# Kernel tuning notes

Measured on AMD Instinct MI355X. Metric: run time of the kernel, lower is better.

## Reference

```python
import jax, jax.numpy as jnp
import numpy as np

N = 100000   # nodes
E = 1600000  # edges (avg degree ~16)
DIN, DH, DOUT = 128, 128, 32
EPS = 1e-5


def setup_inputs() -> dict:
    key = jax.random.key(0)
    ks = jax.random.split(key, 6)
    x = jax.random.normal(ks[0], (N, DIN), jnp.float32)
    edge_index = jax.random.randint(ks[1], (2, E), 0, N, dtype=jnp.int64)

    def w(k, i, o):
        return jax.random.normal(k, (i, o), jnp.float32) * (1.0 / np.sqrt(i))

    return dict(
        x=x, edge_index=edge_index,
        W0=w(ks[2], DIN, DH), b0=jnp.zeros((DH,), jnp.float32),
        g0=jnp.ones((DH,), jnp.float32), be0=jnp.zeros((DH,), jnp.float32),
        W1=w(ks[3], DH, DH), b1=jnp.zeros((DH,), jnp.float32),
        g1=jnp.ones((DH,), jnp.float32), be1=jnp.zeros((DH,), jnp.float32),
        W2=w(ks[4], DH, DOUT), b2=jnp.zeros((DOUT,), jnp.float32),
    )


def _gcn_conv(x, src, dst, norm, W, b, n):
    # x' = scatter_add_dst( norm * (x W)[src] ) + b   (PyG GCNConv, self-loops in src/dst)
    h = x @ W
    out = jax.ops.segment_sum(h[src] * norm[:, None], dst, num_segments=n)
    return out + b


def _bn(x, g, b):
    # training-mode BatchNorm1d over the node axis (biased variance)
    m = x.mean(axis=0)
    v = jnp.mean((x - m) ** 2, axis=0)
    return (x - m) * jax.lax.rsqrt(v + EPS) * g + b


def reference(x, edge_index, W0, b0, g0, be0, W1, b1, g1, be1, W2, b2):
    n = x.shape[0]
    loops = jnp.arange(n, dtype=edge_index.dtype)
    src = jnp.concatenate([edge_index[0], loops])
    dst = jnp.concatenate([edge_index[1], loops])
    # symmetric degree normalization: deg computed on destination with self-loops
    deg = jax.ops.segment_sum(jnp.ones_like(dst, dtype=x.dtype), dst, num_segments=n)
    dinv = jnp.where(deg > 0, jax.lax.rsqrt(jnp.maximum(deg, 1.0)), 0.0)
    norm = dinv[src] * dinv[dst]  # [E+N]

    h = _gcn_conv(x, src, dst, norm, W0, b0, n)
    h = jax.nn.relu(_bn(h, g0, be0))  # dropout is identity at eval
    h = _gcn_conv(h, src, dst, norm, W1, b1, n)
    h = jax.nn.relu(_bn(h, g1, be1))
    h = _gcn_conv(h, src, dst, norm, W2, b2, n)
    return jax.nn.log_softmax(h, axis=1)
```

## Files before the change

kernel.cpp:

```cpp
#include <hip/hip_runtime.h>
#include <hip/hip_bf16.h>
#include <cstdint>
#include <cstddef>

#define BN_EPS 1e-5f

__global__ void detect_k(const int* __restrict__ edges, int* __restrict__ flag) {
    int t = threadIdx.x;
    int v = edges[2 * t + 1];
    unsigned long long b = __ballot(v == 0);
    if (t == 0) flag[0] = (b == ~0ULL) ? 1 : 0;
}

__global__ void init_k(int* __restrict__ cnt, float* __restrict__ stats, int n) {
    int i = blockIdx.x * 256 + threadIdx.x;
    if (i < n) cnt[i] = 0;
    if (i < 1024) stats[i] = 0.0f;
}

__global__ void convert_count_k(const void* __restrict__ edges, int E, const int* __restrict__ flag,
                                int* __restrict__ src32, int* __restrict__ dst32,
                                int* __restrict__ ord, int* __restrict__ cnt) {
    int e = blockIdx.x * 256 + threadIdx.x;
    if (e >= E) return;
    int s, d;
    if (flag[0]) {
        const long long* p = (const long long*)edges;
        s = (int)p[e]; d = (int)p[(size_t)E + e];
    } else {
        const int* p = (const int*)edges;
        s = p[e]; d = p[(size_t)E + e];
    }
    src32[e] = s; dst32[e] = d;
    ord[e] = atomicAdd(&cnt[d], 1);
}

__global__ __launch_bounds__(256) void scan1_k(const int* __restrict__ cnt,
                                               int* __restrict__ stmp,
                                               int* __restrict__ bsum, int n) {
    __shared__ int lds[256];
    int t = threadIdx.x, b = blockIdx.x;
    int base = b * 1024 + t * 4;
    int v0 = (base + 0 < n) ? cnt[base + 0] : 0;
    int v1 = (base + 1 < n) ? cnt[base + 1] : 0;
    int v2 = (base + 2 < n) ? cnt[base + 2] : 0;
    int v3 = (base + 3 < n) ? cnt[base + 3] : 0;
    int p0 = v0, p1 = p0 + v1, p2 = p1 + v2, p3 = p2 + v3;
    lds[t] = p3;
    __syncthreads();
    int own = p3;
    for (int o = 1; o < 256; o <<= 1) {
        int x = (t >= o) ? lds[t - o] : 0;
        __syncthreads();
        lds[t] += x;
        __syncthreads();
    }
    int excl = lds[t] - own;
    if (base + 0 < n) stmp[base + 0] = excl + p0;
    if (base + 1 < n) stmp[base + 1] = excl + p1;
    if (base + 2 < n) stmp[base + 2] = excl + p2;
    if (base + 3 < n) stmp[base + 3] = excl + p3;
    if (t == 255) bsum[b] = lds[255];
}

__global__ void scan2_k(int* __restrict__ bsum, int nb) {
    __shared__ int lds[128];
    int t = threadIdx.x;
    int v = (t < nb) ? bsum[t] : 0;
    lds[t] = v;
    __syncthreads();
    for (int o = 1; o < 128; o <<= 1) {
        int x = (t >= o) ? lds[t - o] : 0;
        __syncthreads();
        lds[t] += x;
        __syncthreads();
    }
    if (t < nb) bsum[t] = lds[t] - v;
}

__global__ void scan3_k(const int* __restrict__ cnt, const int* __restrict__ stmp,
                        const int* __restrict__ bsum, int* __restrict__ rowptr,
                        float* __restrict__ dinv, int n, int E) {
    int i = blockIdx.x * 256 + threadIdx.x;
    if (i < n) {
        rowptr[i] = stmp[i] - cnt[i] + bsum[i >> 10];
        dinv[i] = rsqrtf((float)(cnt[i] + 1));
    }
    if (i == 0) rowptr[n] = E;
}

__global__ void fill_k(const int* __restrict__ src32, const int* __restrict__ dst32,
                       const int* __restrict__ ord, const int* __restrict__ rowptr,
                       const float* __restrict__ dinv,
                       int2* __restrict__ csre, int E) {
    int e = blockIdx.x * 256 + threadIdx.x;
    if (e >= E) return;
    int s = src32[e], d = dst32[e];
    int slot = rowptr[d] + ord[e];
    float w = dinv[s] * dinv[d];
    csre[slot] = make_int2(s, __float_as_int(w));
}

__device__ inline unsigned pack_bf16(float a, float b) {
    unsigned ua = __float_as_uint(a);
    unsigned ub = __float_as_uint(b);
    ua += 0x7FFFu + ((ua >> 16) & 1u);
    ub += 0x7FFFu + ((ub >> 16) & 1u);
    return (ua >> 16) | (ub & 0xFFFF0000u);
}

__device__ inline void unp_bf16(unsigned u, float& a, float& b) {
    a = __uint_as_float(u << 16);
    b = __uint_as_float(u & 0xFFFF0000u);
}

template <int NCOL, bool FUSE_BN, bool OUT_BF16>
__global__ __launch_bounds__(256) void gemm_k(const float* __restrict__ X,
                                              const float* __restrict__ W,
                                              void* __restrict__ Yv, int nrows,
                                              const float* __restrict__ stats,
                                              const float* __restrict__ gam,
                                              const float* __restrict__ bet) {
    constexpr int KDIM = 128;
    constexpr int TM = 64;
    constexpr int KT = 32;
    constexpr int CPT = NCOL / 16;
    __shared__ float xt[KDIM][TM + 4];
    __shared__ float wt[KT][NCOL];

    const int t = threadIdx.x;
    const int ty = t >> 4, tx = t & 15;
    const int row0 = blockIdx.x * TM;

    float sc[4], sh[4];
    if (FUSE_BN) {
        float invn = 1.0f / (float)nrows;
        int k4c = (t & 31) * 4;
#pragma unroll
        for (int j = 0; j < 4; ++j) {
            int c = k4c + j;
            float m = stats[c] * invn;
            float var = stats[128 + c] * invn - m * m;
            float s = rsqrtf(var + BN_EPS) * gam[c];
            sc[j] = s;
            sh[j] = bet[c] - m * s;
        }
    }

    const float4* X4 = (const float4*)X;
#pragma unroll
    for (int i = 0; i < 8; ++i) {
        int idx = i * 256 + t;
        int r = idx >> 5;
        int k4 = idx & 31;
        int gr = row0 + r;
        if (gr > nrows - 1) gr = nrows - 1;
        float4 v = X4[(size_t)gr * 32 + k4];
        if (FUSE_BN) {
            v.x = fmaxf(fmaf(v.x, sc[0], sh[0]), 0.0f);
            v.y = fmaxf(fmaf(v.y, sc[1], sh[1]), 0.0f);
            v.z = fmaxf(fmaf(v.z, sc[2], sh[2]), 0.0f);
            v.w = fmaxf(fmaf(v.w, sc[3], sh[3]), 0.0f);
        }
        xt[k4 * 4 + 0][r] = v.x;
        xt[k4 * 4 + 1][r] = v.y;
        xt[k4 * 4 + 2][r] = v.z;
        xt[k4 * 4 + 3][r] = v.w;
    }

    int colIdx[CPT];
#pragma unroll
    for (int c = 0; c < CPT; ++c)
        colIdx[c] = OUT_BF16 ? (2 * tx + (c & 1) + 32 * (c >> 1)) : (tx + 16 * c);

    float acc[4][CPT];
#pragma unroll
    for (int r = 0; r < 4; ++r)
#pragma unroll
        for (int c = 0; c < CPT; ++c) acc[r][c] = 0.0f;

    const float4* W4 = (const float4*)W;
    for (int kt = 0; kt < KDIM / KT; ++kt) {
        __syncthreads();
        constexpr int F4 = KT * NCOL / 4;
#pragma unroll
        for (int i = 0; i < F4 / 256; ++i) {
            int idx = i * 256 + t;
            int r = idx / (NCOL / 4);
            int c4 = idx % (NCOL / 4);
            float4 v = W4[(size_t)(kt * KT + r) * (NCOL / 4) + c4];
            *(float4*)&wt[r][c4 * 4] = v;
        }
        __syncthreads();
#pragma unroll
        for (int k = 0; k < KT; ++k) {
            float4 a = *(const float4*)&xt[kt * KT + k][ty * 4];
            float av[4] = {a.x, a.y, a.z, a.w};
            float bv[CPT];
#pragma unroll
            for (int c = 0; c < CPT; ++c) bv[c] = wt[k][colIdx[c]];
#pragma unroll
            for (int r = 0; r < 4; ++r)
#pragma unroll
                for (int c = 0; c < CPT; ++c)
                    acc[r][c] = fmaf(av[r], bv[c], acc[r][c]);
        }
    }

#pragma unroll
    for (int r = 0; r < 4; ++r) {
        int gr = row0 + ty * 4 + r;
        if (gr < nrows) {
            if (OUT_BF16) {
                unsigned* Y16 = (unsigned*)Yv;
#pragma unroll
                for (int c2 = 0; c2 < CPT / 2; ++c2)
                    Y16[(size_t)gr * (NCOL / 2) + tx + 16 * c2] =
                        pack_bf16(acc[r][2 * c2], acc[r][2 * c2 + 1]);
            } else {
                float* Y = (float*)Yv;
#pragma unroll
                for (int c = 0; c < CPT; ++c)
                    Y[(size_t)gr * NCOL + tx + 16 * c] = acc[r][c];
            }
        }
    }
}

__global__ __launch_bounds__(256) void agg16_k(const unsigned* __restrict__ H16,
                                               const float* __restrict__ dinv,
                                               const int* __restrict__ rowptr,
                                               const int2* __restrict__ csre,
                                               const float* __restrict__ bias,
                                               float* __restrict__ out, int n) {
    int g = threadIdx.x >> 4;
    int lane = threadIdx.x & 15;
    int node = blockIdx.x * 16 + g;
    if (node >= n) return;

    const uint4* H4 = (const uint4*)H16;
    float di = dinv[node];
    float w0 = di * di;
    float acc[8];
    {
        uint4 sv = H4[(size_t)node * 16 + lane];
        float a, b;
        unp_bf16(sv.x, a, b); acc[0] = w0 * a; acc[1] = w0 * b;
        unp_bf16(sv.y, a, b); acc[2] = w0 * a; acc[3] = w0 * b;
        unp_bf16(sv.z, a, b); acc[4] = w0 * a; acc[5] = w0 * b;
        unp_bf16(sv.w, a, b); acc[6] = w0 * a; acc[7] = w0 * b;
    }

    int s = rowptr[node], e = rowptr[node + 1];
    for (; s + 1 < e; s += 2) {
        int2 ev0 = csre[s];
        int2 ev1 = csre[s + 1];
        uint4 h0 = H4[(size_t)ev0.x * 16 + lane];
        uint4 h1 = H4[(size_t)ev1.x * 16 + lane];
        float wa = __int_as_float(ev0.y);
        float wb = __int_as_float(ev1.y);
        float a, b;
        unp_bf16(h0.x, a, b); acc[0] = fmaf(wa, a, acc[0]); acc[1] = fmaf(wa, b, acc[1]);
        unp_bf16(h0.y, a, b); acc[2] = fmaf(wa, a, acc[2]); acc[3] = fmaf(wa, b, acc[3]);
        unp_bf16(h0.z, a, b); acc[4] = fmaf(wa, a, acc[4]); acc[5] = fmaf(wa, b, acc[5]);
        unp_bf16(h0.w, a, b); acc[6] = fmaf(wa, a, acc[6]); acc[7] = fmaf(wa, b, acc[7]);
        unp_bf16(h1.x, a, b); acc[0] = fmaf(wb, a, acc[0]); acc[1] = fmaf(wb, b, acc[1]);
        unp_bf16(h1.y, a, b); acc[2] = fmaf(wb, a, acc[2]); acc[3] = fmaf(wb, b, acc[3]);
        unp_bf16(h1.z, a, b); acc[4] = fmaf(wb, a, acc[4]); acc[5] = fmaf(wb, b, acc[5]);
        unp_bf16(h1.w, a, b); acc[6] = fmaf(wb, a, acc[6]); acc[7] = fmaf(wb, b, acc[7]);
    }
    if (s < e) {
        int2 ev = csre[s];
        uint4 hv = H4[(size_t)ev.x * 16 + lane];
        float w = __int_as_float(ev.y);
        float a, b;
        unp_bf16(hv.x, a, b); acc[0] = fmaf(w, a, acc[0]); acc[1] = fmaf(w, b, acc[1]);
        unp_bf16(hv.y, a, b); acc[2] = fmaf(w, a, acc[2]); acc[3] = fmaf(w, b, acc[3]);
        unp_bf16(hv.z, a, b); acc[4] = fmaf(w, a, acc[4]); acc[5] = fmaf(w, b, acc[5]);
        unp_bf16(hv.w, a, b); acc[6] = fmaf(w, a, acc[6]); acc[7] = fmaf(w, b, acc[7]);
    }

    const float4* B4 = (const float4*)bias;
    float4 b0 = B4[2 * lane], b1 = B4[2 * lane + 1];
    float4* O4 = (float4*)out;
    O4[(size_t)node * 32 + 2 * lane] =
        make_float4(acc[0] + b0.x, acc[1] + b0.y, acc[2] + b0.z, acc[3] + b0.w);
    O4[(size_t)node * 32 + 2 * lane + 1] =
        make_float4(acc[4] + b1.x, acc[5] + b1.y, acc[6] + b1.z, acc[7] + b1.w);
}

template <int F4>
__global__ __launch_bounds__(256) void agg_k(const float* __restrict__ H,
                                             const float* __restrict__ dinv,
                                             const int* __restrict__ rowptr,
                                             const int2* __restrict__ csre,
                                             const float* __restrict__ bias,
                                             float* __restrict__ out, int n) {
    constexpr int GP = 256 / F4;
    int g = threadIdx.x / F4;
    int lane = threadIdx.x % F4;
    int node = blockIdx.x * GP + g;
    if (node >= n) return;

    const float4* H4 = (const float4*)H;
    float di = dinv[node];
    float w0 = di * di;
    float4 v = H4[(size_t)node * F4 + lane];
    float ax = v.x * w0, ay = v.y * w0, az = v.z * w0, aw = v.w * w0;

    int s = rowptr[node], e = rowptr[node + 1];
    for (; s + 3 < e; s += 4) {
        int2 ev0 = csre[s];
        int2 ev1 = csre[s + 1];
        int2 ev2 = csre[s + 2];
        int2 ev3 = csre[s + 3];
        float4 h0 = H4[(size_t)ev0.x * F4 + lane];
        float4 h1 = H4[(size_t)ev1.x * F4 + lane];
        float4 h2 = H4[(size_t)ev2.x * F4 + lane];
        float4 h3 = H4[(size_t)ev3.x * F4 + lane];
        float wa = __int_as_float(ev0.y);
        float wb = __int_as_float(ev1.y);
        float wc = __int_as_float(ev2.y);
        float wd = __int_as_float(ev3.y);
        ax = fmaf(wa, h0.x, ax); ay = fmaf(wa, h0.y, ay);
        az = fmaf(wa, h0.z, az); aw = fmaf(wa, h0.w, aw);
        ax = fmaf(wb, h1.x, ax); ay = fmaf(wb, h1.y, ay);
        az = fmaf(wb, h1.z, az); aw = fmaf(wb, h1.w, aw);
        ax = fmaf(wc, h2.x, ax); ay = fmaf(wc, h2.y, ay);
        az = fmaf(wc, h2.z, az); aw = fmaf(wc, h2.w, aw);
        ax = fmaf(wd, h3.x, ax); ay = fmaf(wd, h3.y, ay);
        az = fmaf(wd, h3.z, az); aw = fmaf(wd, h3.w, aw);
    }
    for (; s < e; ++s) {
        int2 ev = csre[s];
        float w = __int_as_float(ev.y);
        float4 hv = H4[(size_t)ev.x * F4 + lane];
        ax = fmaf(w, hv.x, ax);
        ay = fmaf(w, hv.y, ay);
        az = fmaf(w, hv.z, az);
        aw = fmaf(w, hv.w, aw);
    }
    float4 b4 = ((const float4*)bias)[lane];
    float4 o = make_float4(ax + b4.x, ay + b4.y, az + b4.z, aw + b4.w);
    ((float4*)out)[(size_t)node * F4 + lane] = o;
}

__global__ __launch_bounds__(256) void bnstats_k(const float* __restrict__ X,
                                                 float* __restrict__ stats, int n) {
    __shared__ float ls[256], ls2[256];
    int t = threadIdx.x;
    int col = t & 127;
    int half = t >> 7;
    float s = 0.0f, s2 = 0.0f;
    for (int r = blockIdx.x * 2 + half; r < n; r += gridDim.x * 2) {
        float v = X[(size_t)r * 128 + col];
        s += v;
        s2 = fmaf(v, v, s2);
    }
    ls[t] = s; ls2[t] = s2;
    __syncthreads();
    if (t < 128) {
        s = ls[t] + ls[t + 128];
        s2 = ls2[t] + ls2[t + 128];
        atomicAdd(&stats[col], s);
        atomicAdd(&stats[128 + col], s2);
    }
}

__global__ __launch_bounds__(256) void lsm_k(const float* __restrict__ X,
                                             float* __restrict__ out, int n) {
    int t = threadIdx.x;
    int g = t >> 5;
    int lane = t & 31;
    int row = blockIdx.x * 8 + g;
    if (row >= n) return;
    float v = X[(size_t)row * 32 + lane];
    float m = v;
    for (int o = 16; o; o >>= 1) m = fmaxf(m, __shfl_xor(m, o, 32));
    float ex = __expf(v - m);
    float s = ex;
    for (int o = 16; o; o >>= 1) s += __shfl_xor(s, o, 32);
    out[(size_t)row * 32 + lane] = v - m - logf(s);
}

extern "C" void kernel_launch(void* const* d_in, const int* in_sizes, int n_in,
                              void* d_out, int out_size, void* d_ws, size_t ws_size,
                              hipStream_t stream) {
    const int N = in_sizes[0] / 128;
    const int E = in_sizes[1] / 2;

    const float* x   = (const float*)d_in[0];
    const void*  edg = d_in[1];
    const float* W0  = (const float*)d_in[2];
    const float* b0  = (const float*)d_in[3];
    const float* g0  = (const float*)d_in[4];
    const float* be0 = (const float*)d_in[5];
    const float* W1  = (const float*)d_in[6];
    const float* b1  = (const float*)d_in[7];
    const float* g1  = (const float*)d_in[8];
    const float* be1 = (const float*)d_in[9];
    const float* W2  = (const float*)d_in[10];
    const float* b2  = (const float*)d_in[11];
    float* out = (float*)d_out;

    char* ws = (char*)d_ws;
    size_t off = 0;
    auto alloc = [&](size_t bytes) {
        char* p = ws + off;
        off = (off + bytes + 255) & ~(size_t)255;
        return p;
    };
    int*   flag   = (int*)  alloc(16);
    float* dinv   = (float*)alloc((size_t)N * 4);
    int*   cnt    = (int*)  alloc((size_t)N * 4);
    int*   src32  = (int*)  alloc((size_t)E * 4);
    int*   dst32  = (int*)  alloc((size_t)E * 4);
    int*   ord    = (int*)  alloc((size_t)E * 4);
    int*   rowptr = (int*)  alloc((size_t)(N + 1) * 4);
    int*   stmp   = (int*)  alloc((size_t)N * 4);
    int*   bsum   = (int*)  alloc(512);
    int2*  csre   = (int2*) alloc((size_t)E * 8);
    float* h      = (float*)alloc((size_t)N * 128 * 4);
    float* agg    = (float*)alloc((size_t)N * 128 * 4);
    float* stats  = (float*)alloc(1024 * 4);
    float* stats0 = stats;
    float* stats1 = stats + 256;
    unsigned* h16 = (unsigned*)h;
    (void)ws_size; (void)n_in; (void)out_size;

    dim3 B(256);
    int gN   = (N + 255) / 256;
    int gE   = (E + 255) / 256;
    int nb   = (N + 1023) / 1024;
    int gGm  = (N + 63) / 64;
    int gA16 = (N + 15) / 16;
    int gA8  = (N + 31) / 32;
    int gLSM = (N + 7) / 8;

    detect_k<<<dim3(1), dim3(64), 0, stream>>>((const int*)edg, flag);
    init_k<<<gN, B, 0, stream>>>(cnt, stats, N);
    convert_count_k<<<gE, B, 0, stream>>>(edg, E, flag, src32, dst32, ord, cnt);
    scan1_k<<<nb, B, 0, stream>>>(cnt, stmp, bsum, N);
    scan2_k<<<dim3(1), dim3(128), 0, stream>>>(bsum, nb);
    scan3_k<<<gN, B, 0, stream>>>(cnt, stmp, bsum, rowptr, dinv, N, E);
    fill_k<<<gE, B, 0, stream>>>(src32, dst32, ord, rowptr, dinv, csre, E);

    gemm_k<128, false, true><<<gGm, B, 0, stream>>>(x, W0, h16, N, nullptr, nullptr, nullptr);
    agg16_k<<<gA16, B, 0, stream>>>(h16, dinv, rowptr, csre, b0, agg, N);
    bnstats_k<<<dim3(512), B, 0, stream>>>(agg, stats0, N);

    gemm_k<128, true, true><<<gGm, B, 0, stream>>>(agg, W1, h16, N, stats0, g0, be0);
    agg16_k<<<gA16, B, 0, stream>>>(h16, dinv, rowptr, csre, b1, agg, N);
    bnstats_k<<<dim3(512), B, 0, stream>>>(agg, stats1, N);

    gemm_k<32, true, false><<<gGm, B, 0, stream>>>(agg, W2, h, N, stats1, g1, be1);
    agg_k<8><<<gA8, B, 0, stream>>>(h, dinv, rowptr, csre, b2, agg, N);
    lsm_k<<<gLSM, B, 0, stream>>>(agg, out, N);
}
```

Before: 623.5 us.

## Use bf16 MFMA for 128-wide GEMMs and pad degree counters

Replaces the FP32 SIMT GEMM for the two 128x128 layers with a bf16 MFMA kernel. Inputs are converted to bf16 into swizzled LDS tiles, and a small pre-pass transposes each weight matrix and packs it into bf16. Separately, the per-node degree counters are spread to one every 32 ints so that atomics on different nodes do not contend on the same cache line. The MFMA path rounds GEMM inputs to bf16, which lowers precision. The padded counters also make the count array much larger, adding init and scan traffic.

```diff
diff --git a/kernel.cpp b/kernel.cpp
--- a/kernel.cpp
+++ b/kernel.cpp
@@ -4,6 +4,10 @@
 #include <cstddef>
 
 #define BN_EPS 1e-5f
+#define CNTS 32
+
+typedef __attribute__((ext_vector_type(8))) short bf16x8;
+typedef __attribute__((ext_vector_type(4))) float f32x4;
 
 __global__ void detect_k(const int* __restrict__ edges, int* __restrict__ flag) {
     int t = threadIdx.x;
@@ -12,9 +16,9 @@
     if (t == 0) flag[0] = (b == ~0ULL) ? 1 : 0;
 }
 
-__global__ void init_k(int* __restrict__ cnt, float* __restrict__ stats, int n) {
+__global__ void init_k(int* __restrict__ cnt, float* __restrict__ stats, int n32) {
     int i = blockIdx.x * 256 + threadIdx.x;
-    if (i < n) cnt[i] = 0;
+    if (i < n32) cnt[i] = 0;
     if (i < 1024) stats[i] = 0.0f;
 }
 
@@ -32,7 +36,7 @@
         s = p[e]; d = p[(size_t)E + e];
     }
     src32[e] = s; dst32[e] = d;
-    ord[e] = atomicAdd(&cnt[d], 1);
+    ord[e] = atomicAdd(&cnt[d * CNTS], 1);
 }
 
 __global__ __launch_bounds__(256) void scan1_k(const int* __restrict__ cnt,
@@ -41,10 +45,10 @@
     __shared__ int lds[256];
     int t = threadIdx.x, b = blockIdx.x;
     int base = b * 1024 + t * 4;
-    int v0 = (base + 0 < n) ? cnt[base + 0] : 0;
-    int v1 = (base + 1 < n) ? cnt[base + 1] : 0;
-    int v2 = (base + 2 < n) ? cnt[base + 2] : 0;
-    int v3 = (base + 3 < n) ? cnt[base + 3] : 0;
+    int v0 = (base + 0 < n) ? cnt[(base + 0) * CNTS] : 0;
+    int v1 = (base + 1 < n) ? cnt[(base + 1) * CNTS] : 0;
+    int v2 = (base + 2 < n) ? cnt[(base + 2) * CNTS] : 0;
+    int v3 = (base + 3 < n) ? cnt[(base + 3) * CNTS] : 0;
     int p0 = v0, p1 = p0 + v1, p2 = p1 + v2, p3 = p2 + v3;
     lds[t] = p3;
     __syncthreads();
@@ -83,8 +87,9 @@
                         float* __restrict__ dinv, int n, int E) {
     int i = blockIdx.x * 256 + threadIdx.x;
     if (i < n) {
-        rowptr[i] = stmp[i] - cnt[i] + bsum[i >> 10];
-        dinv[i] = rsqrtf((float)(cnt[i] + 1));
+        int c = cnt[i * CNTS];
+        rowptr[i] = stmp[i] - c + bsum[i >> 10];
+        dinv[i] = rsqrtf((float)(c + 1));
     }
     if (i == 0) rowptr[n] = E;
 }
@@ -114,10 +119,113 @@
     b = __uint_as_float(u & 0xFFFF0000u);
 }
 
-template <int NCOL, bool FUSE_BN, bool OUT_BF16>
+__global__ void wprep_k(const float* __restrict__ W, unsigned* __restrict__ Wt16) {
+    int idx = blockIdx.x * 256 + threadIdx.x;
+    int j = idx >> 7;
+    int c = idx & 127;
+    float a = W[(size_t)(2 * j) * 128 + c];
+    float b = W[(size_t)(2 * j + 1) * 128 + c];
+    Wt16[(size_t)c * 64 + j] = pack_bf16(a, b);
+}
+
+template <bool FUSE_BN>
+__global__ __launch_bounds__(256) void gemm_mfma_k(const float* __restrict__ X,
+                                                   const unsigned* __restrict__ Wt16,
+                                                   unsigned* __restrict__ Y16, int nrows,
+                                                   const float* __restrict__ stats,
+                                                   const float* __restrict__ gam,
+                                                   const float* __restrict__ bet) {
+    __shared__ __align__(16) char lds[(64 + 128) * 256];
+    char* Alds = lds;
+    char* Blds = lds + 64 * 256;
+
+    const int t = threadIdx.x;
+    const int lane = t & 63;
+    const int wid = t >> 6;
+    const int row0 = blockIdx.x * 64;
+
+    float sc[8], sh[8];
+    if (FUSE_BN) {
+        float invn = 1.0f / (float)nrows;
+        int c0 = (t & 15) * 8;
+#pragma unroll
+        for (int j = 0; j < 8; ++j) {
+            int c = c0 + j;
+            float m = stats[c] * invn;
+            float var = stats[128 + c] * invn - m * m;
+            float s = rsqrtf(var + BN_EPS) * gam[c];
+            sc[j] = s;
+            sh[j] = bet[c] - m * s;
+        }
+    }
+
+    const float4* X4 = (const float4*)X;
+    const int kg = t & 15;
+#pragma unroll
+    for (int i = 0; i < 4; ++i) {
+        int r = i * 16 + (t >> 4);
+        int gr = row0 + r;
+        if (gr > nrows - 1) gr = nrows - 1;
+        float4 v0 = X4[(size_t)gr * 32 + kg * 2];
+        float4 v1 = X4[(size_t)gr * 32 + kg * 2 + 1];
+        float f[8] = {v0.x, v0.y, v0.z, v0.w, v1.x, v1.y, v1.z, v1.w};
+        if (FUSE_BN) {
+#pragma unroll
+            for (int j = 0; j < 8; ++j) f[j] = fmaxf(fmaf(f[j], sc[j], sh[j]), 0.0f);
+        }
+        uint4 p = make_uint4(pack_bf16(f[0], f[1]), pack_bf16(f[2], f[3]),
+                             pack_bf16(f[4], f[5]), pack_bf16(f[6], f[7]));
+        int byte = (r * 256 + kg * 16) ^ ((r & 7) << 4);
+        *(uint4*)(Alds + byte) = p;
+    }
+    const uint4* Wg4 = (const uint4*)Wt16;
+#pragma unroll
+    for (int i = 0; i < 8; ++i) {
+        int idx = i * 256 + t;
+        int wr = idx >> 4;
+        uint4 v = Wg4[idx];
+        int byte = (wr * 256 + (idx & 15) * 16) ^ ((wr & 7) << 4);
+        *(uint4*)(Blds + byte) = v;
+    }
+    __syncthreads();
+
+    f32x4 acc[8];
+#pragma unroll
+    for (int ct = 0; ct < 8; ++ct) acc[ct] = (f32x4){0.f, 0.f, 0.f, 0.f};
+
+    const int rA = wid * 16 + (lane & 15);
+    const int g = lane >> 4;
+#pragma unroll
+    for (int kt = 0; kt < 4; ++kt) {
+        int abyte = (rA * 256 + kt * 64 + g * 16) ^ ((rA & 7) << 4);
+        bf16x8 a = *(const bf16x8*)(Alds + abyte);
+#pragma unroll
+        for (int ct = 0; ct < 8; ++ct) {
+            int brow = ct * 16 + (lane & 15);
+            int bbyte = (brow * 256 + kt * 64 + g * 16) ^ ((brow & 7) << 4);
+            bf16x8 b = *(const bf16x8*)(Blds + bbyte);
+            acc[ct] = __builtin_amdgcn_mfma_f32_16x16x32_bf16(a, b, acc[ct], 0, 0, 0);
+        }
+    }
+
+    const int c = lane & 15;
+#pragma unroll
+    for (int ct = 0; ct < 8; ++ct) {
+#pragma unroll
+        for (int r = 0; r < 4; ++r) {
+            float own = acc[ct][r];
+            float oth = __shfl_xor(own, 1);
+            int gr = row0 + wid * 16 + (lane >> 4) * 4 + r;
+            if (!(c & 1) && gr < nrows)
+                Y16[(size_t)gr * 64 + (ct * 16 + c) / 2] = pack_bf16(own, oth);
+        }
+    }
+}
+
+template <int NCOL, bool FUSE_BN>
 __global__ __launch_bounds__(256) void gemm_k(const float* __restrict__ X,
                                               const float* __restrict__ W,
-                                              void* __restrict__ Yv, int nrows,
+                                              float* __restrict__ Y, int nrows,
                                               const float* __restrict__ stats,
                                               const float* __restrict__ gam,
                                               const float* __restrict__ bet) {
@@ -168,11 +276,6 @@
         xt[k4 * 4 + 3][r] = v.w;
     }
 
-    int colIdx[CPT];
-#pragma unroll
-    for (int c = 0; c < CPT; ++c)
-        colIdx[c] = OUT_BF16 ? (2 * tx + (c & 1) + 32 * (c >> 1)) : (tx + 16 * c);
-
     float acc[4][CPT];
 #pragma unroll
     for (int r = 0; r < 4; ++r)
@@ -198,7 +301,7 @@
             float av[4] = {a.x, a.y, a.z, a.w};
             float bv[CPT];
 #pragma unroll
-            for (int c = 0; c < CPT; ++c) bv[c] = wt[k][colIdx[c]];
+            for (int c = 0; c < CPT; ++c) bv[c] = wt[k][tx + 16 * c];
 #pragma unroll
             for (int r = 0; r < 4; ++r)
 #pragma unroll
@@ -211,18 +314,9 @@
     for (int r = 0; r < 4; ++r) {
         int gr = row0 + ty * 4 + r;
         if (gr < nrows) {
-            if (OUT_BF16) {
-                unsigned* Y16 = (unsigned*)Yv;
-#pragma unroll
-                for (int c2 = 0; c2 < CPT / 2; ++c2)
-                    Y16[(size_t)gr * (NCOL / 2) + tx + 16 * c2] =
-                        pack_bf16(acc[r][2 * c2], acc[r][2 * c2 + 1]);
-            } else {
-                float* Y = (float*)Yv;
-#pragma unroll
-                for (int c = 0; c < CPT; ++c)
-                    Y[(size_t)gr * NCOL + tx + 16 * c] = acc[r][c];
-            }
+#pragma unroll
+            for (int c = 0; c < CPT; ++c)
+                Y[(size_t)gr * NCOL + tx + 16 * c] = acc[r][c];
         }
     }
 }
@@ -410,27 +504,29 @@
         off = (off + bytes + 255) & ~(size_t)255;
         return p;
     };
-    int*   flag   = (int*)  alloc(16);
-    float* dinv   = (float*)alloc((size_t)N * 4);
-    int*   cnt    = (int*)  alloc((size_t)N * 4);
-    int*   src32  = (int*)  alloc((size_t)E * 4);
-    int*   dst32  = (int*)  alloc((size_t)E * 4);
-    int*   ord    = (int*)  alloc((size_t)E * 4);
-    int*   rowptr = (int*)  alloc((size_t)(N + 1) * 4);
-    int*   stmp   = (int*)  alloc((size_t)N * 4);
-    int*   bsum   = (int*)  alloc(512);
-    int2*  csre   = (int2*) alloc((size_t)E * 8);
-    float* h      = (float*)alloc((size_t)N * 128 * 4);
-    float* agg    = (float*)alloc((size_t)N * 128 * 4);
-    float* stats  = (float*)alloc(1024 * 4);
-    float* stats0 = stats;
-    float* stats1 = stats + 256;
-    unsigned* h16 = (unsigned*)h;
+    int*      flag   = (int*)     alloc(16);
+    float*    dinv   = (float*)   alloc((size_t)N * 4);
+    int*      cnt    = (int*)     alloc((size_t)N * CNTS * 4);
+    int*      src32  = (int*)     alloc((size_t)E * 4);
+    int*      dst32  = (int*)     alloc((size_t)E * 4);
+    int*      ord    = (int*)     alloc((size_t)E * 4);
+    int*      rowptr = (int*)     alloc((size_t)(N + 1) * 4);
+    int*      stmp   = (int*)     alloc((size_t)N * 4);
+    int*      bsum   = (int*)     alloc(512);
+    int2*     csre   = (int2*)    alloc((size_t)E * 8);
+    float*    h      = (float*)   alloc((size_t)N * 128 * 4);
+    float*    agg    = (float*)   alloc((size_t)N * 128 * 4);
+    float*    stats  = (float*)   alloc(1024 * 4);
+    unsigned* wt16   = (unsigned*)alloc(128 * 64 * 4);
+    float*    stats0 = stats;
+    float*    stats1 = stats + 256;
+    unsigned* h16    = (unsigned*)h;
     (void)ws_size; (void)n_in; (void)out_size;
 
     dim3 B(256);
+    int gE   = (E + 255) / 256;
     int gN   = (N + 255) / 256;
-    int gE   = (E + 255) / 256;
+    int gNC  = (N * CNTS + 255) / 256;
     int nb   = (N + 1023) / 1024;
     int gGm  = (N + 63) / 64;
     int gA16 = (N + 15) / 16;
@@ -438,22 +534,24 @@
     int gLSM = (N + 7) / 8;
 
     detect_k<<<dim3(1), dim3(64), 0, stream>>>((const int*)edg, flag);
-    init_k<<<gN, B, 0, stream>>>(cnt, stats, N);
+    init_k<<<gNC, B, 0, stream>>>(cnt, stats, N * CNTS);
     convert_count_k<<<gE, B, 0, stream>>>(edg, E, flag, src32, dst32, ord, cnt);
     scan1_k<<<nb, B, 0, stream>>>(cnt, stmp, bsum, N);
     scan2_k<<<dim3(1), dim3(128), 0, stream>>>(bsum, nb);
     scan3_k<<<gN, B, 0, stream>>>(cnt, stmp, bsum, rowptr, dinv, N, E);
     fill_k<<<gE, B, 0, stream>>>(src32, dst32, ord, rowptr, dinv, csre, E);
 
-    gemm_k<128, false, true><<<gGm, B, 0, stream>>>(x, W0, h16, N, nullptr, nullptr, nullptr);
+    wprep_k<<<dim3(32), B, 0, stream>>>(W0, wt16);
+    gemm_mfma_k<false><<<gGm, B, 0, stream>>>(x, wt16, h16, N, nullptr, nullptr, nullptr);
     agg16_k<<<gA16, B, 0, stream>>>(h16, dinv, rowptr, csre, b0, agg, N);
     bnstats_k<<<dim3(512), B, 0, stream>>>(agg, stats0, N);
 
-    gemm_k<128, true, true><<<gGm, B, 0, stream>>>(agg, W1, h16, N, stats0, g0, be0);
+    wprep_k<<<dim3(32), B, 0, stream>>>(W1, wt16);
+    gemm_mfma_k<true><<<gGm, B, 0, stream>>>(agg, wt16, h16, N, stats0, g0, be0);
     agg16_k<<<gA16, B, 0, stream>>>(h16, dinv, rowptr, csre, b1, agg, N);
     bnstats_k<<<dim3(512), B, 0, stream>>>(agg, stats1, N);
 
-    gemm_k<32, true, false><<<gGm, B, 0, stream>>>(agg, W2, h, N, stats1, g1, be1);
+    gemm_k<32, true><<<gGm, B, 0, stream>>>(agg, W2, h, N, stats1, g1, be1);
     agg_k<8><<<gA8, B, 0, stream>>>(h, dinv, rowptr, csre, b2, agg, N);
     lsm_k<<<gLSM, B, 0, stream>>>(agg, out, N);
 }
```

Result: faster. 550.5 us (-11.7%).
